# Kernel tuning notes

Hardware: AMD Instinct MI355X
Metric: run time of the kernel (lower is better)

Reference implementation:

```python
import jax, jax.numpy as jnp
import numpy as np

N_NODES = 100000
N_HEDGES = 25000
N_EDGES = 1000000
NUM_GRAPHS = 64
H = 64


def _seg_mean(vals, idx, num_segments):
    s = jax.ops.segment_sum(vals, idx, num_segments=num_segments)
    cnt = jax.ops.segment_sum(jnp.ones((vals.shape[0],), vals.dtype), idx, num_segments=num_segments)
    return s / jnp.maximum(cnt, 1.0)[:, None]


def _sage(x_src, x_dst, src, dst, Wl, bl, Wr):
    # gather src features per edge, scatter-mean to dst, then lin_l(agg)+lin_r(x_dst)
    agg = _seg_mean(x_src[src], dst, x_dst.shape[0])
    return agg @ Wl + bl + x_dst @ Wr


def setup_inputs() -> dict:
    key = jax.random.key(0)
    ks = jax.random.split(key, 32)
    d = {}
    d['node_x'] = jax.random.normal(ks[0], (N_NODES, 1), jnp.float32)
    d['edge_x'] = jax.random.normal(ks[1], (N_HEDGES, 2), jnp.float32)
    d['n2e_src'] = jax.random.randint(ks[2], (N_EDGES,), 0, N_NODES)
    d['n2e_dst'] = jax.random.randint(ks[3], (N_EDGES,), 0, N_HEDGES)
    d['e2n_src'] = jax.random.randint(ks[4], (N_EDGES,), 0, N_HEDGES)
    d['e2n_dst'] = jax.random.randint(ks[5], (N_EDGES,), 0, N_NODES)
    d['node_batch'] = jnp.sort(jax.random.randint(ks[6], (N_NODES,), 0, NUM_GRAPHS))
    d['edge_batch'] = jnp.sort(jax.random.randint(ks[7], (N_HEDGES,), 0, NUM_GRAPHS))
    def w(k, shape, fan_in):
        return jax.random.normal(k, shape, jnp.float32) / np.sqrt(fan_in)
    d['Wn'] = w(ks[8], (1, H), 1); d['bn'] = jnp.zeros((H,), jnp.float32)
    d['We'] = w(ks[9], (2, H), 2); d['be'] = jnp.zeros((H,), jnp.float32)
    names = ['1l_n2e', '1r_n2e', '1l_e2n', '1r_e2n', '2l_n2e', '2r_n2e', '2l_e2n', '2r_e2n']
    for i, nm in enumerate(names):
        d['W' + nm] = w(ks[10 + i], (H, H), H)
        if 'l' in nm.split('_')[0]:
            d['b' + nm] = jnp.zeros((H,), jnp.float32)
    d['Wout'] = w(ks[20], (2 * H, 32), 2 * H)
    d['bout'] = jnp.zeros((32,), jnp.float32)
    return d


def reference(node_x, edge_x, n2e_src, n2e_dst, e2n_src, e2n_dst, node_batch, edge_batch,
              Wn, bn, We, be,
              W1l_n2e, b1l_n2e, W1r_n2e, W1l_e2n, b1l_e2n, W1r_e2n,
              W2l_n2e, b2l_n2e, W2r_n2e, W2l_e2n, b2l_e2n, W2r_e2n,
              Wout, bout):
    xn = jax.nn.relu(node_x @ Wn + bn)      # [N, H]
    xe = jax.nn.relu(edge_x @ We + be)      # [E_h, H]
    # HeteroConv layer 1 (each dst type has exactly one incoming edge type)
    xe1 = jax.nn.relu(_sage(xn, xe, n2e_src, n2e_dst, W1l_n2e, b1l_n2e, W1r_n2e))
    xn1 = jax.nn.relu(_sage(xe, xn, e2n_src, e2n_dst, W1l_e2n, b1l_e2n, W1r_e2n))
    # HeteroConv layer 2
    xe2 = jax.nn.relu(_sage(xn1, xe1, n2e_src, n2e_dst, W2l_n2e, b2l_n2e, W2r_n2e))
    xn2 = jax.nn.relu(_sage(xe1, xn1, e2n_src, e2n_dst, W2l_e2n, b2l_e2n, W2r_e2n))
    node_pool = _seg_mean(xn2, node_batch, NUM_GRAPHS)  # [G, H]
    edge_pool = _seg_mean(xe2, edge_batch, NUM_GRAPHS)  # [G, H]
    combined = jnp.concatenate([node_pool, edge_pool], axis=-1)  # [G, 2H]
    return combined @ Wout + bout  # [G, 32]
```

## Files before the change

kernel.cpp:

```cpp
#include <hip/hip_runtime.h>

#define N_NODES 100000
#define N_HEDGES 25000
#define N_EDGES 1000000
#define NG 64
#define HD 64

#define EB_SH 8
#define EB_NB 98
#define EB_CAP 12000
#define NB_SH 9
#define NB_NB 196
#define NB_CAP 6200
#define TILE 4096
#define TPS 245
#define ENC_F4 ((N_NODES + N_HEDGES) * 16)

typedef __attribute__((ext_vector_type(4))) float f4;
typedef __attribute__((ext_vector_type(4))) unsigned short us4;
typedef __attribute__((ext_vector_type(8))) unsigned short us8;
typedef __attribute__((ext_vector_type(8))) short s8b;

__device__ __forceinline__ unsigned short f2bf(float f) {
    unsigned int u = __float_as_uint(f);
    unsigned int r = (u + 0x7FFFu + ((u >> 16) & 1u)) >> 16;
    return (unsigned short)r;
}
__device__ __forceinline__ float bf2f(unsigned short h) {
    return __uint_as_float((unsigned int)h << 16);
}
__device__ __forceinline__ us4 f4_to_bf4(f4 v) {
    us4 h;
    h[0] = f2bf(v[0]); h[1] = f2bf(v[1]); h[2] = f2bf(v[2]); h[3] = f2bf(v[3]);
    return h;
}

__global__ __launch_bounds__(256) void prep(
    const float* __restrict__ W1lE, const float* __restrict__ W1rE,
    const float* __restrict__ W1lN, const float* __restrict__ W1rN,
    const float* __restrict__ W2lE, const float* __restrict__ W2rE,
    const float* __restrict__ W2lN, const float* __restrict__ W2rN,
    unsigned short* __restrict__ WtH, int* __restrict__ zbase, int zn) {
    int b = blockIdx.x, t = threadIdx.x;
    if (b < 4) {
        const float *Wl, *Wr;
        switch (b) {
            case 0: Wl = W1lE; Wr = W1rE; break;
            case 1: Wl = W1lN; Wr = W1rN; break;
            case 2: Wl = W2lE; Wr = W2rE; break;
            default: Wl = W2lN; Wr = W2rN; break;
        }
        unsigned short* o = WtH + b * 8192;
        for (int idx = t; idx < 8192; idx += 256) {
            int c = idx >> 7, k = idx & 127;
            float v = (k < 64) ? Wl[k * 64 + c] : Wr[(k - 64) * 64 + c];
            o[c * 128 + k] = f2bf(v);
        }
    } else {
        int i = (b - 4) * 256 + t;
        if (i < zn) zbase[i] = 0;
    }
}

__global__ __launch_bounds__(256) void bin_encode(
    const int* __restrict__ n2e_src, const int* __restrict__ n2e_dst,
    const int* __restrict__ e2n_src, const int* __restrict__ e2n_dst,
    int* __restrict__ binE, int* __restrict__ binN,
    int* __restrict__ gcntE, int* __restrict__ gcntN,
    const float* __restrict__ node_x, const float* __restrict__ edge_x,
    const float* __restrict__ Wn, const float* __restrict__ bn,
    const float* __restrict__ We, const float* __restrict__ be,
    unsigned short* __restrict__ xnH, unsigned short* __restrict__ xeH) {
    __shared__ int pairsL[TILE];
    __shared__ int hist[256], scanv[256], start[256], curs[256], gbase[256];
    int t = threadIdx.x;
    if ((int)blockIdx.x >= 2 * TPS) {
        int i4 = ((int)blockIdx.x - 2 * TPS) * 256 + t;
        if (i4 < N_NODES * 16) {
            int row = i4 >> 4, fq = i4 & 15;
            f4 wn = *(const f4*)(Wn + fq * 4);
            f4 bnv = *(const f4*)(bn + fq * 4);
            float xv = node_x[row];
            f4 v;
#pragma unroll
            for (int c = 0; c < 4; c++) v[c] = fmaxf(xv * wn[c] + bnv[c], 0.f);
            *(us4*)(xnH + (long)i4 * 4) = f4_to_bf4(v);
        } else if (i4 < ENC_F4) {
            int j = i4 - N_NODES * 16;
            int row = j >> 4, fq = j & 15;
            f4 w0 = *(const f4*)(We + fq * 4);
            f4 w1 = *(const f4*)(We + HD + fq * 4);
            f4 bev = *(const f4*)(be + fq * 4);
            float x0 = edge_x[2 * row], x1 = edge_x[2 * row + 1];
            f4 v;
#pragma unroll
            for (int c = 0; c < 4; c++) v[c] = fmaxf(x0 * w0[c] + x1 * w1[c] + bev[c], 0.f);
            *(us4*)(xeH + (long)j * 4) = f4_to_bf4(v);
        }
        return;
    }
    int side = (int)blockIdx.x >= TPS;
    int lb = blockIdx.x - (side ? TPS : 0);
    const int* dsts = side ? e2n_dst : n2e_dst;
    const int* srcs = side ? e2n_src : n2e_src;
    int NB = side ? NB_NB : EB_NB;
    int SH = side ? NB_SH : EB_SH;
    int CAP = side ? NB_CAP : EB_CAP;
    int* bins = side ? binN : binE;
    int* gcnt = side ? gcntN : gcntE;
    int base = lb * TILE;

    hist[t] = 0;
    __syncthreads();

    int pair[16], buck[16];
#pragma unroll
    for (int k = 0; k < 16; k++) {
        int e = base + k * 256 + t;
        if (e < N_EDGES) {
            int d = dsts[e];
            int s = srcs[e];
            buck[k] = d >> SH;
            pair[k] = ((d & ((1 << SH) - 1)) << 17) | s;
            atomicAdd(&hist[buck[k]], 1);
        } else buck[k] = -1;
    }
    __syncthreads();
    int v = hist[t];
    scanv[t] = v;
    __syncthreads();
    for (int o = 1; o < 256; o <<= 1) {
        int x = (t >= o) ? scanv[t - o] : 0;
        __syncthreads();
        scanv[t] += x;
        __syncthreads();
    }
    start[t] = scanv[t] - v;
    curs[t] = scanv[t] - v;
    if (t < NB && v > 0) gbase[t] = t * CAP + atomicAdd(&gcnt[t], v);
    __syncthreads();
    int total = scanv[255];
#pragma unroll
    for (int k = 0; k < 16; k++) {
        if (buck[k] >= 0) {
            int slot = atomicAdd(&curs[buck[k]], 1);
            pairsL[slot] = pair[k];
        }
    }
    __syncthreads();
    for (int i = t; i < total; i += 256) {
        int lo = 0, hi = NB - 1;
        while (lo < hi) { int mid = (lo + hi + 1) >> 1; if (start[mid] <= i) lo = mid; else hi = mid - 1; }
        bins[gbase[lo] + (i - start[lo])] = pairsL[i];
    }
}

__global__ __launch_bounds__(512) void fine_fill(
    const int* __restrict__ binE, const int* __restrict__ binN,
    const int* __restrict__ gcntE, const int* __restrict__ gcntN,
    int* __restrict__ off, int* __restrict__ deg,
    int* __restrict__ srtE, unsigned short* __restrict__ srtN) {
    __shared__ int hist[512], scanv[512];
    int t = threadIdx.x;
    int side = (int)blockIdx.x >= EB_NB;
    int b = blockIdx.x - (side ? EB_NB : 0);
    int NROWS = side ? 512 : 256;
    int CAP = side ? NB_CAP : EB_CAP;
    const int* bins = (side ? binN : binE) + (long)b * CAP;
    int cnt_b = (side ? gcntN : gcntE)[b];
    int rowbase = side ? (N_HEDGES + b * 512) : b * 256;
    int nrows = (side ? N_NODES : N_HEDGES) - (side ? b * 512 : b * 256);
    if (nrows > NROWS) nrows = NROWS;
    int* srtEb = srtE + (long)b * CAP;
    unsigned short* srtNb = srtN + (long)b * CAP;

    hist[t] = 0;
    __syncthreads();
    for (int i = t; i < cnt_b; i += 512) atomicAdd(&hist[bins[i] >> 17], 1);
    __syncthreads();
    int v = hist[t];
    scanv[t] = v;
    __syncthreads();
    for (int o = 1; o < 512; o <<= 1) {
        int x = (t >= o) ? scanv[t - o] : 0;
        __syncthreads();
        scanv[t] += x;
        __syncthreads();
    }
    int excl = scanv[t] - v;
    if (t < nrows) { off[rowbase + t] = b * CAP + excl; deg[rowbase + t] = v; }
    scanv[t] = excl;
    __syncthreads();
    for (int i = t; i < cnt_b; i += 512) {
        int p = bins[i];
        int pos = atomicAdd(&scanv[p >> 17], 1);
        if (side) srtNb[pos] = (unsigned short)(p & 0x1FFFF);
        else srtEb[pos] = p & 0x1FFFF;
    }
}

__global__ __launch_bounds__(256) void gather_layer(
    const unsigned short* __restrict__ xnH, const unsigned short* __restrict__ xeH,
    const int* __restrict__ off, const int* __restrict__ deg,
    const int* __restrict__ srtE, const unsigned short* __restrict__ srtN,
    unsigned short* __restrict__ aggEH, unsigned short* __restrict__ aggNH) {
    int lane = threadIdx.x & 63;
    int w = blockIdx.x * 4 + (threadIdx.x >> 6);
    int NW = gridDim.x * 4;
    int sub = lane >> 3;
    int fq = lane & 7;
    const int RT = N_HEDGES + N_NODES;
    for (int r = w; r < RT; r += NW) {
        const unsigned short* xsrc; unsigned short* agg; int rr;
        bool eSide = r < N_HEDGES;
        if (eSide) { rr = r; xsrc = xnH; agg = aggEH; }
        else { rr = r - N_HEDGES; xsrc = xeH; agg = aggNH; }
        int lo = off[r];
        int dg = deg[r];
        f4 a0 = {0.f, 0.f, 0.f, 0.f}, a1 = a0, b0 = a0, b1 = a0;
        for (int j0 = 0; j0 < dg; j0 += 64) {
            int chunk = dg - j0;
            if (chunk > 64) chunk = 64;
            int idv;
            if (eSide) idv = (j0 + lane < dg) ? srtE[lo + j0 + lane] : 0;
            else idv = (j0 + lane < dg) ? (int)srtN[lo + j0 + lane] : 0;
            int jj = 0;
            for (; jj + 16 <= chunk; jj += 16) {
                int s0 = __shfl(idv, jj + sub);
                int s1 = __shfl(idv, jj + 8 + sub);
                us8 h0 = *(const us8*)(xsrc + (long)s0 * HD + fq * 8);
                us8 h1 = *(const us8*)(xsrc + (long)s1 * HD + fq * 8);
#pragma unroll
                for (int i = 0; i < 4; i++) {
                    a0[i] += bf2f(h0[i]); a1[i] += bf2f(h0[i + 4]);
                    b0[i] += bf2f(h1[i]); b1[i] += bf2f(h1[i + 4]);
                }
            }
            for (; jj < chunk; jj += 8) {
                int e = jj + sub;
                int s = __shfl(idv, e & 63);
                us8 h = *(const us8*)(xsrc + (long)s * HD + fq * 8);
                if (e < chunk) {
#pragma unroll
                    for (int i = 0; i < 4; i++) { a0[i] += bf2f(h[i]); a1[i] += bf2f(h[i + 4]); }
                }
            }
        }
        a0 += b0; a1 += b1;
#pragma unroll
        for (int m = 8; m <= 32; m <<= 1) {
#pragma unroll
            for (int i = 0; i < 4; i++) {
                a0[i] += __shfl_xor(a0[i], m);
                a1[i] += __shfl_xor(a1[i], m);
            }
        }
        if (sub == 0) {
            float invd = 1.f / (float)(dg > 1 ? dg : 1);
            us4 p0 = f4_to_bf4(a0 * invd), p1 = f4_to_bf4(a1 * invd);
            us8 o;
#pragma unroll
            for (int i = 0; i < 4; i++) { o[i] = p0[i]; o[i + 4] = p1[i]; }
            *(us8*)(agg + (long)rr * HD + fq * 8) = o;
        }
    }
}

__global__ __launch_bounds__(256) void combine_mfma(
    const unsigned short* __restrict__ aggEH, const unsigned short* __restrict__ xeH,
    const unsigned short* __restrict__ aggNH, const unsigned short* __restrict__ xnH,
    const unsigned short* __restrict__ WtE, const float* __restrict__ blE,
    const unsigned short* __restrict__ WtN, const float* __restrict__ blN,
    unsigned short* __restrict__ outEH, unsigned short* __restrict__ outNH, int gbE) {
    __shared__ unsigned short sA[64][136];
    __shared__ unsigned short sW[64][136];
    int t = threadIdx.x;
    const unsigned short *aggH, *xdstH, *Wt;
    const float* bl;
    unsigned short* outH;
    int rows, row0;
    if ((int)blockIdx.x < gbE) {
        aggH = aggEH; xdstH = xeH; Wt = WtE; bl = blE; outH = outEH;
        rows = N_HEDGES; row0 = blockIdx.x * 64;
    } else {
        aggH = aggNH; xdstH = xnH; Wt = WtN; bl = blN; outH = outNH;
        rows = N_NODES; row0 = (blockIdx.x - gbE) * 64;
    }

#pragma unroll
    for (int q = 0; q < 4; q++) {
        int idx = q * 256 + t;
        int c = idx >> 4, ch = idx & 15;
        *(us8*)&sW[c][ch * 8] = *(const us8*)(Wt + c * 128 + ch * 8);
    }
#pragma unroll
    for (int q = 0; q < 4; q++) {
        int idx = q * 256 + t;
        int r = idx >> 4, ch = idx & 15;
        int gr = row0 + r;
        us8 v;
        if (gr < rows) {
            v = (ch < 8) ? *(const us8*)(aggH + (long)gr * HD + ch * 8)
                         : *(const us8*)(xdstH + (long)gr * HD + (ch - 8) * 8);
        } else {
            v = (us8){0, 0, 0, 0, 0, 0, 0, 0};
        }
        *(us8*)&sA[r][ch * 8] = v;
    }
    __syncthreads();

    int lane = t & 63, w = t >> 6;
    int m0 = w * 16;
    int l15 = lane & 15, quad = lane >> 4;
    f4 acc[4];
#pragma unroll
    for (int ct = 0; ct < 4; ct++) {
        float b = bl[ct * 16 + l15];
        acc[ct] = (f4){b, b, b, b};
    }
#pragma unroll
    for (int kb = 0; kb < 4; kb++) {
        s8b a = *(const s8b*)&sA[m0 + l15][kb * 32 + quad * 8];
#pragma unroll
        for (int ct = 0; ct < 4; ct++) {
            s8b bfr = *(const s8b*)&sW[ct * 16 + l15][kb * 32 + quad * 8];
            acc[ct] = __builtin_amdgcn_mfma_f32_16x16x32_bf16(a, bfr, acc[ct], 0, 0, 0);
        }
    }
#pragma unroll
    for (int ct = 0; ct < 4; ct++) {
#pragma unroll
        for (int r = 0; r < 4; r++) {
            int gr = row0 + m0 + quad * 4 + r;
            if (gr < rows) outH[(long)gr * HD + ct * 16 + l15] = f2bf(fmaxf(acc[ct][r], 0.f));
        }
    }
}

__device__ __forceinline__ int lower_bound_dev(const int* arr, int n, int key) {
    int lo = 0, hi = n;
    while (lo < hi) { int mid = (lo + hi) >> 1; if (arr[mid] < key) lo = mid + 1; else hi = mid; }
    return lo;
}

#define PB_N 8
#define PB_E 2
__global__ __launch_bounds__(256) void pool_bf(
    const unsigned short* __restrict__ xnH, const unsigned short* __restrict__ xeH,
    const int* __restrict__ node_batch, const int* __restrict__ edge_batch,
    float* __restrict__ poolN, float* __restrict__ poolE) {
    __shared__ float sp[4][64];
    int b = blockIdx.x;
    const unsigned short* x; const int* batch; float* pool; int n, g, part, P;
    if (b < NG * PB_N) { x = xnH; batch = node_batch; pool = poolN; n = N_NODES; g = b / PB_N; part = b % PB_N; P = PB_N; }
    else { b -= NG * PB_N; x = xeH; batch = edge_batch; pool = poolE; n = N_HEDGES; g = b / PB_E; part = b % PB_E; P = PB_E; }
    int s = lower_bound_dev(batch, n, g);
    int e = lower_bound_dev(batch, n, g + 1);
    int len = e - s;
    int start = s + (int)(((long)len * part) / P);
    int end = s + (int)(((long)len * (part + 1)) / P);
    int lane = threadIdx.x & 63, w = threadIdx.x >> 6;
    int fq = lane & 7, sub = lane >> 3;
    f4 a0 = {0.f, 0.f, 0.f, 0.f}, a1 = a0;
    for (int r = start + w * 8 + sub; r < end; r += 32) {
        us8 h = *(const us8*)(x + (long)r * HD + fq * 8);
#pragma unroll
        for (int c = 0; c < 4; c++) { a0[c] += bf2f(h[c]); a1[c] += bf2f(h[c + 4]); }
    }
#pragma unroll
    for (int c = 0; c < 4; c++) {
        a0[c] += __shfl_xor(a0[c], 8);  a1[c] += __shfl_xor(a1[c], 8);
        a0[c] += __shfl_xor(a0[c], 16); a1[c] += __shfl_xor(a1[c], 16);
        a0[c] += __shfl_xor(a0[c], 32); a1[c] += __shfl_xor(a1[c], 32);
    }
    if (lane < 8) {
        *(f4*)&sp[w][fq * 8] = a0;
        *(f4*)&sp[w][fq * 8 + 4] = a1;
    }
    __syncthreads();
    if (threadIdx.x < 64) {
        int tt = threadIdx.x;
        float v = sp[0][tt] + sp[1][tt] + sp[2][tt] + sp[3][tt];
        if (v != 0.f) atomicAdd(&pool[g * HD + tt], v);
    }
}

__global__ __launch_bounds__(64) void final_readout(
    const float* __restrict__ poolN, const float* __restrict__ poolE,
    const int* __restrict__ node_batch, const int* __restrict__ edge_batch,
    const float* __restrict__ Wout, const float* __restrict__ bout,
    float* __restrict__ out) {
    __shared__ float inv[2];
    int g = blockIdx.x, t = threadIdx.x;
    if (t < 2) {
        const int* arr = t ? edge_batch : node_batch;
        int n = t ? N_HEDGES : N_NODES;
        int lo = lower_bound_dev(arr, n, g);
        int hi = lower_bound_dev(arr, n, g + 1);
        int c = hi - lo;
        inv[t] = 1.f / (float)(c > 1 ? c : 1);
    }
    __syncthreads();
    if (t < 32) {
        float iN = inv[0], iE = inv[1];
        float s = bout[t];
#pragma unroll 8
        for (int k = 0; k < HD; k++)
            s += poolN[g * HD + k] * iN * Wout[k * 32 + t]
               + poolE[g * HD + k] * iE * Wout[(HD + k) * 32 + t];
        out[g * 32 + t] = s;
    }
}

extern "C" void kernel_launch(void* const* d_in, const int* in_sizes, int n_in,
                              void* d_out, int out_size, void* d_ws, size_t ws_size,
                              hipStream_t stream) {
    const float* node_x = (const float*)d_in[0];
    const float* edge_x = (const float*)d_in[1];
    const int* n2e_src = (const int*)d_in[2];
    const int* n2e_dst = (const int*)d_in[3];
    const int* e2n_src = (const int*)d_in[4];
    const int* e2n_dst = (const int*)d_in[5];
    const int* node_batch = (const int*)d_in[6];
    const int* edge_batch = (const int*)d_in[7];
    const float* Wn = (const float*)d_in[8];
    const float* bn = (const float*)d_in[9];
    const float* We = (const float*)d_in[10];
    const float* be = (const float*)d_in[11];
    const float* W1l_n2e = (const float*)d_in[12];
    const float* b1l_n2e = (const float*)d_in[13];
    const float* W1r_n2e = (const float*)d_in[14];
    const float* W1l_e2n = (const float*)d_in[15];
    const float* b1l_e2n = (const float*)d_in[16];
    const float* W1r_e2n = (const float*)d_in[17];
    const float* W2l_n2e = (const float*)d_in[18];
    const float* b2l_n2e = (const float*)d_in[19];
    const float* W2r_n2e = (const float*)d_in[20];
    const float* W2l_e2n = (const float*)d_in[21];
    const float* b2l_e2n = (const float*)d_in[22];
    const float* W2r_e2n = (const float*)d_in[23];
    const float* Wout = (const float*)d_in[24];
    const float* bout = (const float*)d_in[25];
    float* out = (float*)d_out;

    unsigned short* AH0 = (unsigned short*)d_ws;
    unsigned short* BH0 = AH0 + N_NODES * HD;
    unsigned short* AH1 = BH0 + N_HEDGES * HD;
    unsigned short* BH1 = AH1 + N_NODES * HD;
    unsigned short* aggNH = BH1 + N_HEDGES * HD;
    unsigned short* aggEH = aggNH + N_NODES * HD;
    unsigned short* WtH = aggEH + N_HEDGES * HD;
    float* poolN = (float*)(WtH + 4 * 8192);
    float* poolE = poolN + NG * HD;
    int* gcntE = (int*)(poolE + NG * HD);
    int* gcntN = gcntE + EB_NB;
    int* off = gcntN + NB_NB;
    int* deg = off + (N_HEDGES + N_NODES);
    int* binE = deg + (N_HEDGES + N_NODES);
    int* binN = binE + EB_NB * EB_CAP;
    int* srtE = binN + NB_NB * NB_CAP;
    unsigned short* srtN = (unsigned short*)(srtE + EB_NB * EB_CAP);

    const int Bt = 256;

    int zn = 2 * NG * HD + EB_NB + NB_NB;
    prep<<<4 + (zn + Bt - 1) / Bt, Bt, 0, stream>>>(
        W1l_n2e, W1r_n2e, W1l_e2n, W1r_e2n,
        W2l_n2e, W2r_n2e, W2l_e2n, W2r_e2n,
        WtH, (int*)poolN, zn);

    int encBlocks = (ENC_F4 + Bt - 1) / Bt;
    bin_encode<<<2 * TPS + encBlocks, Bt, 0, stream>>>(
        n2e_src, n2e_dst, e2n_src, e2n_dst, binE, binN, gcntE, gcntN,
        node_x, edge_x, Wn, bn, We, be, AH0, BH0);

    fine_fill<<<EB_NB + NB_NB, 512, 0, stream>>>(binE, binN, gcntE, gcntN,
                                                 off, deg, srtE, srtN);

    int gbE = (N_HEDGES + 63) / 64;
    int gbN = (N_NODES + 63) / 64;
    int gridC = gbE + gbN;

    gather_layer<<<2048, Bt, 0, stream>>>(AH0, BH0, off, deg, srtE, srtN, aggEH, aggNH);
    combine_mfma<<<gridC, Bt, 0, stream>>>(aggEH, BH0, aggNH, AH0,
                                           WtH, b1l_n2e, WtH + 8192, b1l_e2n,
                                           BH1, AH1, gbE);

    gather_layer<<<2048, Bt, 0, stream>>>(AH1, BH1, off, deg, srtE, srtN, aggEH, aggNH);
    combine_mfma<<<gridC, Bt, 0, stream>>>(aggEH, BH1, aggNH, AH1,
                                           WtH + 16384, b2l_n2e, WtH + 24576, b2l_e2n,
                                           BH0, AH0, gbE);

    pool_bf<<<NG * PB_N + NG * PB_E, Bt, 0, stream>>>(AH0, BH0, node_batch, edge_batch, poolN, poolE);

    final_readout<<<NG, 64, 0, stream>>>(poolN, poolE, node_batch, edge_batch, Wout, bout, out);
}
```

Measured before the change: 201.7 us.

## Switch intermediate features from bf16 to fp16 with packed half accumulation in gather

Feature buffers, weights and MFMA inputs change from bf16 to fp16. The gather kernel now accumulates neighbour sums directly in packed half (h4) vectors instead of converting to fp32, and loads 8-byte chunks with 16 lanes per row and 4 rows per wavefront step. This removes the bf16-to-fp32 conversion ALU work and halves accumulator registers and shuffle traffic. In exchange, summing up to roughly 40 neighbours in fp16 gives lower precision and a risk of overflow, and the narrower per-lane loads may reduce memory-level parallelism.

Result: faster. 184.1 us (-8.7%).

```diff
diff --git a/kernel.cpp b/kernel.cpp
--- a/kernel.cpp
+++ b/kernel.cpp
@@ -17,22 +17,15 @@
 #define ENC_F4 ((N_NODES + N_HEDGES) * 16)
 
 typedef __attribute__((ext_vector_type(4))) float f4;
-typedef __attribute__((ext_vector_type(4))) unsigned short us4;
-typedef __attribute__((ext_vector_type(8))) unsigned short us8;
-typedef __attribute__((ext_vector_type(8))) short s8b;
-
-__device__ __forceinline__ unsigned short f2bf(float f) {
-    unsigned int u = __float_as_uint(f);
-    unsigned int r = (u + 0x7FFFu + ((u >> 16) & 1u)) >> 16;
-    return (unsigned short)r;
-}
-__device__ __forceinline__ float bf2f(unsigned short h) {
-    return __uint_as_float((unsigned int)h << 16);
-}
-__device__ __forceinline__ us4 f4_to_bf4(f4 v) {
-    us4 h;
-    h[0] = f2bf(v[0]); h[1] = f2bf(v[1]); h[2] = f2bf(v[2]); h[3] = f2bf(v[3]);
-    return h;
+typedef __attribute__((ext_vector_type(4))) _Float16 h4;
+typedef __attribute__((ext_vector_type(8))) _Float16 h8;
+typedef __attribute__((ext_vector_type(2))) int i2;
+
+__device__ __forceinline__ h4 f4_to_h4(f4 v) {
+    h4 o;
+    o[0] = (_Float16)v[0]; o[1] = (_Float16)v[1];
+    o[2] = (_Float16)v[2]; o[3] = (_Float16)v[3];
+    return o;
 }
 
 __global__ __launch_bounds__(256) void prep(
@@ -40,7 +33,7 @@
     const float* __restrict__ W1lN, const float* __restrict__ W1rN,
     const float* __restrict__ W2lE, const float* __restrict__ W2rE,
     const float* __restrict__ W2lN, const float* __restrict__ W2rN,
-    unsigned short* __restrict__ WtH, int* __restrict__ zbase, int zn) {
+    _Float16* __restrict__ WtH, int* __restrict__ zbase, int zn) {
     int b = blockIdx.x, t = threadIdx.x;
     if (b < 4) {
         const float *Wl, *Wr;
@@ -50,11 +43,11 @@
             case 2: Wl = W2lE; Wr = W2rE; break;
             default: Wl = W2lN; Wr = W2rN; break;
         }
-        unsigned short* o = WtH + b * 8192;
+        _Float16* o = WtH + b * 8192;
         for (int idx = t; idx < 8192; idx += 256) {
             int c = idx >> 7, k = idx & 127;
             float v = (k < 64) ? Wl[k * 64 + c] : Wr[(k - 64) * 64 + c];
-            o[c * 128 + k] = f2bf(v);
+            o[c * 128 + k] = (_Float16)v;
         }
     } else {
         int i = (b - 4) * 256 + t;
@@ -70,7 +63,7 @@
     const float* __restrict__ node_x, const float* __restrict__ edge_x,
     const float* __restrict__ Wn, const float* __restrict__ bn,
     const float* __restrict__ We, const float* __restrict__ be,
-    unsigned short* __restrict__ xnH, unsigned short* __restrict__ xeH) {
+    _Float16* __restrict__ xnH, _Float16* __restrict__ xeH) {
     __shared__ int pairsL[TILE];
     __shared__ int hist[256], scanv[256], start[256], curs[256], gbase[256];
     int t = threadIdx.x;
@@ -84,7 +77,7 @@
             f4 v;
 #pragma unroll
             for (int c = 0; c < 4; c++) v[c] = fmaxf(xv * wn[c] + bnv[c], 0.f);
-            *(us4*)(xnH + (long)i4 * 4) = f4_to_bf4(v);
+            *(h4*)(xnH + (long)i4 * 4) = f4_to_h4(v);
         } else if (i4 < ENC_F4) {
             int j = i4 - N_NODES * 16;
             int row = j >> 4, fq = j & 15;
@@ -95,7 +88,7 @@
             f4 v;
 #pragma unroll
             for (int c = 0; c < 4; c++) v[c] = fmaxf(x0 * w0[c] + x1 * w1[c] + bev[c], 0.f);
-            *(us4*)(xeH + (long)j * 4) = f4_to_bf4(v);
+            *(h4*)(xeH + (long)j * 4) = f4_to_h4(v);
         }
         return;
     }
@@ -200,24 +193,25 @@
 }
 
 __global__ __launch_bounds__(256) void gather_layer(
-    const unsigned short* __restrict__ xnH, const unsigned short* __restrict__ xeH,
+    const _Float16* __restrict__ xnH, const _Float16* __restrict__ xeH,
     const int* __restrict__ off, const int* __restrict__ deg,
     const int* __restrict__ srtE, const unsigned short* __restrict__ srtN,
-    unsigned short* __restrict__ aggEH, unsigned short* __restrict__ aggNH) {
+    _Float16* __restrict__ aggEH, _Float16* __restrict__ aggNH) {
     int lane = threadIdx.x & 63;
     int w = blockIdx.x * 4 + (threadIdx.x >> 6);
     int NW = gridDim.x * 4;
-    int sub = lane >> 3;
-    int fq = lane & 7;
+    int esub = lane >> 4;
+    int fq = lane & 15;
     const int RT = N_HEDGES + N_NODES;
     for (int r = w; r < RT; r += NW) {
-        const unsigned short* xsrc; unsigned short* agg; int rr;
+        const _Float16* xsrc; _Float16* agg; int rr;
         bool eSide = r < N_HEDGES;
         if (eSide) { rr = r; xsrc = xnH; agg = aggEH; }
         else { rr = r - N_HEDGES; xsrc = xeH; agg = aggNH; }
         int lo = off[r];
         int dg = deg[r];
-        f4 a0 = {0.f, 0.f, 0.f, 0.f}, a1 = a0, b0 = a0, b1 = a0;
+        h4 a0 = {(_Float16)0.f, (_Float16)0.f, (_Float16)0.f, (_Float16)0.f};
+        h4 a1 = a0;
         for (int j0 = 0; j0 < dg; j0 += 64) {
             int chunk = dg - j0;
             if (chunk > 64) chunk = 64;
@@ -225,59 +219,51 @@
             if (eSide) idv = (j0 + lane < dg) ? srtE[lo + j0 + lane] : 0;
             else idv = (j0 + lane < dg) ? (int)srtN[lo + j0 + lane] : 0;
             int jj = 0;
-            for (; jj + 16 <= chunk; jj += 16) {
-                int s0 = __shfl(idv, jj + sub);
-                int s1 = __shfl(idv, jj + 8 + sub);
-                us8 h0 = *(const us8*)(xsrc + (long)s0 * HD + fq * 8);
-                us8 h1 = *(const us8*)(xsrc + (long)s1 * HD + fq * 8);
-#pragma unroll
-                for (int i = 0; i < 4; i++) {
-                    a0[i] += bf2f(h0[i]); a1[i] += bf2f(h0[i + 4]);
-                    b0[i] += bf2f(h1[i]); b1[i] += bf2f(h1[i + 4]);
-                }
+            for (; jj + 8 <= chunk; jj += 8) {
+                int s0 = __shfl(idv, jj + esub);
+                int s1 = __shfl(idv, jj + 4 + esub);
+                h4 h0 = ((const h4*)(xsrc + (long)s0 * HD))[fq];
+                h4 h1 = ((const h4*)(xsrc + (long)s1 * HD))[fq];
+                a0 += h0;
+                a1 += h1;
             }
-            for (; jj < chunk; jj += 8) {
-                int e = jj + sub;
+            for (; jj < chunk; jj += 4) {
+                int e = jj + esub;
                 int s = __shfl(idv, e & 63);
-                us8 h = *(const us8*)(xsrc + (long)s * HD + fq * 8);
-                if (e < chunk) {
-#pragma unroll
-                    for (int i = 0; i < 4; i++) { a0[i] += bf2f(h[i]); a1[i] += bf2f(h[i + 4]); }
-                }
+                h4 h = ((const h4*)(xsrc + (long)s * HD))[fq];
+                if (e < chunk) a0 += h;
             }
         }
-        a0 += b0; a1 += b1;
-#pragma unroll
-        for (int m = 8; m <= 32; m <<= 1) {
-#pragma unroll
-            for (int i = 0; i < 4; i++) {
-                a0[i] += __shfl_xor(a0[i], m);
-                a1[i] += __shfl_xor(a1[i], m);
-            }
-        }
-        if (sub == 0) {
+        a0 += a1;
+#pragma unroll
+        for (int m = 16; m <= 32; m <<= 1) {
+            i2 wv = __builtin_bit_cast(i2, a0);
+            wv.x = __shfl_xor(wv.x, m);
+            wv.y = __shfl_xor(wv.y, m);
+            a0 += __builtin_bit_cast(h4, wv);
+        }
+        if (lane < 16) {
             float invd = 1.f / (float)(dg > 1 ? dg : 1);
-            us4 p0 = f4_to_bf4(a0 * invd), p1 = f4_to_bf4(a1 * invd);
-            us8 o;
-#pragma unroll
-            for (int i = 0; i < 4; i++) { o[i] = p0[i]; o[i + 4] = p1[i]; }
-            *(us8*)(agg + (long)rr * HD + fq * 8) = o;
+            _Float16 ih = (_Float16)invd;
+            h4 o = a0;
+            o[0] *= ih; o[1] *= ih; o[2] *= ih; o[3] *= ih;
+            *(h4*)(agg + (long)rr * HD + fq * 4) = o;
         }
     }
 }
 
 __global__ __launch_bounds__(256) void combine_mfma(
-    const unsigned short* __restrict__ aggEH, const unsigned short* __restrict__ xeH,
-    const unsigned short* __restrict__ aggNH, const unsigned short* __restrict__ xnH,
-    const unsigned short* __restrict__ WtE, const float* __restrict__ blE,
-    const unsigned short* __restrict__ WtN, const float* __restrict__ blN,
-    unsigned short* __restrict__ outEH, unsigned short* __restrict__ outNH, int gbE) {
-    __shared__ unsigned short sA[64][136];
-    __shared__ unsigned short sW[64][136];
+    const _Float16* __restrict__ aggEH, const _Float16* __restrict__ xeH,
+    const _Float16* __restrict__ aggNH, const _Float16* __restrict__ xnH,
+    const _Float16* __restrict__ WtE, const float* __restrict__ blE,
+    const _Float16* __restrict__ WtN, const float* __restrict__ blN,
+    _Float16* __restrict__ outEH, _Float16* __restrict__ outNH, int gbE) {
+    __shared__ _Float16 sA[64][136];
+    __shared__ _Float16 sW[64][136];
     int t = threadIdx.x;
-    const unsigned short *aggH, *xdstH, *Wt;
+    const _Float16 *aggH, *xdstH, *Wt;
     const float* bl;
-    unsigned short* outH;
+    _Float16* outH;
     int rows, row0;
     if ((int)blockIdx.x < gbE) {
         aggH = aggEH; xdstH = xeH; Wt = WtE; bl = blE; outH = outEH;
@@ -291,21 +277,22 @@
     for (int q = 0; q < 4; q++) {
         int idx = q * 256 + t;
         int c = idx >> 4, ch = idx & 15;
-        *(us8*)&sW[c][ch * 8] = *(const us8*)(Wt + c * 128 + ch * 8);
+        *(h8*)&sW[c][ch * 8] = *(const h8*)(Wt + c * 128 + ch * 8);
     }
 #pragma unroll
     for (int q = 0; q < 4; q++) {
         int idx = q * 256 + t;
         int r = idx >> 4, ch = idx & 15;
         int gr = row0 + r;
-        us8 v;
+        h8 v;
         if (gr < rows) {
-            v = (ch < 8) ? *(const us8*)(aggH + (long)gr * HD + ch * 8)
-                         : *(const us8*)(xdstH + (long)gr * HD + (ch - 8) * 8);
+            v = (ch < 8) ? *(const h8*)(aggH + (long)gr * HD + ch * 8)
+                         : *(const h8*)(xdstH + (long)gr * HD + (ch - 8) * 8);
         } else {
-            v = (us8){0, 0, 0, 0, 0, 0, 0, 0};
-        }
-        *(us8*)&sA[r][ch * 8] = v;
+            v = (h8){(_Float16)0.f, (_Float16)0.f, (_Float16)0.f, (_Float16)0.f,
+                     (_Float16)0.f, (_Float16)0.f, (_Float16)0.f, (_Float16)0.f};
+        }
+        *(h8*)&sA[r][ch * 8] = v;
     }
     __syncthreads();
 
@@ -320,11 +307,11 @@
     }
 #pragma unroll
     for (int kb = 0; kb < 4; kb++) {
-        s8b a = *(const s8b*)&sA[m0 + l15][kb * 32 + quad * 8];
+        h8 a = *(const h8*)&sA[m0 + l15][kb * 32 + quad * 8];
 #pragma unroll
         for (int ct = 0; ct < 4; ct++) {
-            s8b bfr = *(const s8b*)&sW[ct * 16 + l15][kb * 32 + quad * 8];
-            acc[ct] = __builtin_amdgcn_mfma_f32_16x16x32_bf16(a, bfr, acc[ct], 0, 0, 0);
+            h8 bfr = *(const h8*)&sW[ct * 16 + l15][kb * 32 + quad * 8];
+            acc[ct] = __builtin_amdgcn_mfma_f32_16x16x32_f16(a, bfr, acc[ct], 0, 0, 0);
         }
     }
 #pragma unroll
@@ -332,7 +319,7 @@
 #pragma unroll
         for (int r = 0; r < 4; r++) {
             int gr = row0 + m0 + quad * 4 + r;
-            if (gr < rows) outH[(long)gr * HD + ct * 16 + l15] = f2bf(fmaxf(acc[ct][r], 0.f));
+            if (gr < rows) outH[(long)gr * HD + ct * 16 + l15] = (_Float16)fmaxf(acc[ct][r], 0.f);
         }
     }
 }
@@ -346,12 +333,12 @@
 #define PB_N 8
 #define PB_E 2
 __global__ __launch_bounds__(256) void pool_bf(
-    const unsigned short* __restrict__ xnH, const unsigned short* __restrict__ xeH,
+    const _Float16* __restrict__ xnH, const _Float16* __restrict__ xeH,
     const int* __restrict__ node_batch, const int* __restrict__ edge_batch,
     float* __restrict__ poolN, float* __restrict__ poolE) {
     __shared__ float sp[4][64];
     int b = blockIdx.x;
-    const unsigned short* x; const int* batch; float* pool; int n, g, part, P;
+    const _Float16* x; const int* batch; float* pool; int n, g, part, P;
     if (b < NG * PB_N) { x = xnH; batch = node_batch; pool = poolN; n = N_NODES; g = b / PB_N; part = b % PB_N; P = PB_N; }
     else { b -= NG * PB_N; x = xeH; batch = edge_batch; pool = poolE; n = N_HEDGES; g = b / PB_E; part = b % PB_E; P = PB_E; }
     int s = lower_bound_dev(batch, n, g);
@@ -363,9 +350,9 @@
     int fq = lane & 7, sub = lane >> 3;
     f4 a0 = {0.f, 0.f, 0.f, 0.f}, a1 = a0;
     for (int r = start + w * 8 + sub; r < end; r += 32) {
-        us8 h = *(const us8*)(x + (long)r * HD + fq * 8);
-#pragma unroll
-        for (int c = 0; c < 4; c++) { a0[c] += bf2f(h[c]); a1[c] += bf2f(h[c + 4]); }
+        h8 h = *(const h8*)(x + (long)r * HD + fq * 8);
+#pragma unroll
+        for (int c = 0; c < 4; c++) { a0[c] += (float)h[c]; a1[c] += (float)h[c + 4]; }
     }
 #pragma unroll
     for (int c = 0; c < 4; c++) {
@@ -443,13 +430,13 @@
     const float* bout = (const float*)d_in[25];
     float* out = (float*)d_out;
 
-    unsigned short* AH0 = (unsigned short*)d_ws;
-    unsigned short* BH0 = AH0 + N_NODES * HD;
-    unsigned short* AH1 = BH0 + N_HEDGES * HD;
-    unsigned short* BH1 = AH1 + N_NODES * HD;
-    unsigned short* aggNH = BH1 + N_HEDGES * HD;
-    unsigned short* aggEH = aggNH + N_NODES * HD;
-    unsigned short* WtH = aggEH + N_HEDGES * HD;
+    _Float16* AH0 = (_Float16*)d_ws;
+    _Float16* BH0 = AH0 + N_NODES * HD;
+    _Float16* AH1 = BH0 + N_HEDGES * HD;
+    _Float16* BH1 = AH1 + N_NODES * HD;
+    _Float16* aggNH = BH1 + N_HEDGES * HD;
+    _Float16* aggEH = aggNH + N_NODES * HD;
+    _Float16* WtH = aggEH + N_HEDGES * HD;
     float* poolN = (float*)(WtH + 4 * 8192);
     float* poolE = poolN + NG * HD;
     int* gcntE = (int*)(poolE + NG * HD);
```
